# Kernel optimization log

Measured on AMD Instinct MI355X. Metric: run time of the kernel, lower is better.

The kernel has to match this reference:

```python
import jax, jax.numpy as jnp
import numpy as np

B, P = 32, 1024
HID, H, D = 512, 8, 64   # hidden_dim, heads, head_dim
MEM, RANK = 64, 64


def setup_inputs() -> dict:
    key = jax.random.key(0)
    ks = jax.random.split(key, 12)
    s1 = 1.0  # Linear(1, hidden): fan_in = 1 -> torch init bound = 1
    sh = 1.0 / np.sqrt(HID)
    sd = 1.0 / np.sqrt(D)
    return {
        "x":    jax.random.normal(ks[0], (B, P), dtype=jnp.float32),
        # q/k/v: Linear(1, hidden) -> weight (hidden,), bias (hidden,)
        "w_q": jax.random.uniform(ks[1], (HID,), jnp.float32, -s1, s1),
        "b_q": jax.random.uniform(ks[2], (HID,), jnp.float32, -s1, s1),
        "w_k": jax.random.uniform(ks[3], (HID,), jnp.float32, -s1, s1),
        "b_k": jax.random.uniform(ks[4], (HID,), jnp.float32, -s1, s1),
        "w_v": jax.random.uniform(ks[5], (HID,), jnp.float32, -s1, s1),
        "b_v": jax.random.uniform(ks[6], (HID,), jnp.float32, -s1, s1),
        # mem_proj: Linear(head_dim, mem_size, bias=False) -> weight (mem, d)
        "w_mem": jax.random.uniform(ks[7], (MEM, D), jnp.float32, -sd, sd),
        # project_to_U / V: Linear(hidden, rank)
        "w_u":  jax.random.uniform(ks[8], (RANK, HID), jnp.float32, -sh, sh),
        "b_u":  jax.random.uniform(ks[9], (RANK,), jnp.float32, -sh, sh),
        "w_v2": jax.random.uniform(ks[10], (RANK, HID), jnp.float32, -sh, sh),
        "b_v2": jax.random.uniform(ks[11], (RANK,), jnp.float32, -sh, sh),
    }


def reference(x, w_q, b_q, w_k, b_k, w_v, b_v, w_mem, w_u, b_u, w_v2, b_v2):
    Bx, p = x.shape
    xu = x[..., None]                                  # (B, p, 1)
    # Linear(1, hidden) is a scalar broadcast: x * w + b
    def to_heads(w, b):
        y = xu * w + b                                 # (B, p, HID)
        return y.reshape(Bx, p, H, D).transpose(0, 2, 1, 3)  # (B, H, p, D)
    Q = to_heads(w_q, b_q)
    K = to_heads(w_k, b_k)
    V = to_heads(w_v, b_v)

    phi = lambda u: jax.nn.elu(u) + 1.0
    Qf = phi(Q)                                        # (B, H, p, D)
    # memory weights: softmax over the p axis (dim=2)
    W_mem = jax.nn.softmax(jnp.einsum('bhpd,md->bhpm', K, w_mem), axis=2)
    mem_KV = jnp.einsum('bhpm,bhpd->bhmd', W_mem, V)   # (B, H, MEM, D)
    attn = jnp.einsum('bhpd,bhmd->bhpm', Qf, mem_KV)   # (B, H, p, MEM)
    h = jnp.einsum('bhpm,bhmd->bhpd', attn, mem_KV)    # (B, H, p, D)
    h = h.transpose(0, 2, 1, 3).reshape(Bx, p, H * D)  # (B, p, HID)

    U = h @ w_u.T + b_u                                # (B, p, RANK)
    Vp = h @ w_v2.T + b_v2                             # (B, p, RANK)
    coeffs_k = jnp.einsum('bpr,bqr->bpq', U, Vp)       # (B, p, p)
    return coeffs_k
```

## Files before the change

### kernel.cpp

```cpp
#include <hip/hip_runtime.h>
#include <hip/hip_bf16.h>

#define BB 32
#define PP 1024
#define HID 512
#define NH 8
#define DD 64
#define MEM 64
#define RANK 64

typedef float f32x4 __attribute__((ext_vector_type(4)));

#define M_OFF   512
#define G_OFF   18432

__global__ __launch_bounds__(1024) void k_fused(
    const float* __restrict__ x, const float* __restrict__ wq,
    const float* __restrict__ bq, const float* __restrict__ wk,
    const float* __restrict__ wv, const float* __restrict__ bv,
    const float* __restrict__ wmem, const float* __restrict__ wu,
    const float* __restrict__ bu, const float* __restrict__ wv2,
    const float* __restrict__ bv2, float* __restrict__ G,
    float* __restrict__ M17) {
  const int t = threadIdx.x;

  if (blockIdx.x == 256) {
    __shared__ float WU[17 * 64];
    __shared__ float WVt[64 * 17];
    const int r = t >> 4;
    const int dq = t & 15;
    for (int j = 0; j < 17; ++j) {
      float su, sv;
      if (j < 16) {
        const int hh = j & 7;
        const float4 w4 = (j < 8) ? *(const float4*)&wv[hh * DD + dq * 4]
                                  : *(const float4*)&bv[hh * DD + dq * 4];
        const float4 u4 = *(const float4*)&wu[r * HID + hh * DD + dq * 4];
        const float4 v4 = *(const float4*)&wv2[r * HID + hh * DD + dq * 4];
        su = u4.x * w4.x + u4.y * w4.y + u4.z * w4.z + u4.w * w4.w;
        sv = v4.x * w4.x + v4.y * w4.y + v4.z * w4.z + v4.w * w4.w;
      } else {
        su = (dq == 0) ? bu[r] : 0.f;
        sv = (dq == 0) ? bv2[r] : 0.f;
      }
      su += __shfl_xor(su, 1); su += __shfl_xor(su, 2);
      su += __shfl_xor(su, 4); su += __shfl_xor(su, 8);
      sv += __shfl_xor(sv, 1); sv += __shfl_xor(sv, 2);
      sv += __shfl_xor(sv, 4); sv += __shfl_xor(sv, 8);
      if (dq == 0) {
        WU[j * 64 + r] = su;
        WVt[r * 17 + j] = sv;
      }
    }
    __syncthreads();
    if (t < 17 * 17) {
      const int ii = t / 17, jj = t - ii * 17;
      float s = 0.f;
      for (int rr = 0; rr < 64; ++rr) s += WU[ii * 64 + rr] * WVt[rr * 17 + jj];
      M17[t] = s;
    }
    return;
  }

  __shared__ float Tl[MEM];
  __shared__ float sS1, sS2;
  const int b = blockIdx.x >> 3;
  const int h = blockIdx.x & 7;
  const int w = t >> 6;
  const int lane = t & 63;
  const float* xr = x + b * PP;

  const float xv = xr[t];

  float xs[16];
#pragma unroll
  for (int k = 0; k < 16; ++k) xs[k] = xr[lane + k * 64];

  for (int mi = 0; mi < 4; ++mi) {
    const int m = w * 4 + mi;
    float a = wk[h * DD + lane] * wmem[m * DD + lane];
#pragma unroll
    for (int off = 32; off >= 1; off >>= 1) a += __shfl_xor(a, off);

    float mx = -INFINITY;
#pragma unroll
    for (int k = 0; k < 16; ++k) mx = fmaxf(mx, xs[k] * a);
#pragma unroll
    for (int off = 32; off >= 1; off >>= 1) mx = fmaxf(mx, __shfl_xor(mx, off));

    float s = 0.f, sx = 0.f;
#pragma unroll
    for (int k = 0; k < 16; ++k) {
      const float e = __expf(xs[k] * a - mx);
      s += e;
      sx += e * xs[k];
    }
#pragma unroll
    for (int off = 32; off >= 1; off >>= 1) {
      s += __shfl_xor(s, off);
      sx += __shfl_xor(sx, off);
    }
    if (lane == 0) Tl[m] = sx / s;
  }
  __syncthreads();

  if (t < 64) {
    const float v = Tl[t];
    float s1 = v, s2 = v * v;
#pragma unroll
    for (int off = 32; off >= 1; off >>= 1) {
      s1 += __shfl_xor(s1, off);
      s2 += __shfl_xor(s2, off);
    }
    if (t == 0) { sS1 = s1; sS2 = s2; }
  }
  __syncthreads();

  float a1 = 0.f, a0 = 0.f;
#pragma unroll 8
  for (int d = 0; d < DD; ++d) {
    const float q = xv * wq[h * DD + d] + bq[h * DD + d];
    const float ph = (q > 0.f) ? (q + 1.f) : __expf(q);
    a1 += ph * wv[h * DD + d];
    a0 += ph * bv[h * DD + d];
  }
  const float s1 = sS1, s2 = sS2;
  const float c1 = a1 * s2 + a0 * s1;
  const float c2 = a1 * s1 + a0 * (float)MEM;
  G[(b * 16 + h) * PP + t] = c1;
  G[(b * 16 + 8 + h) * PP + t] = c2;
}

__global__ __launch_bounds__(256) void k_coeffs(
    const float* __restrict__ G, const float* __restrict__ M17,
    float* __restrict__ out) {
  __shared__ float Ml[17 * 17];
  __shared__ float Gp[16 * 128];
  __shared__ float Gq[16 * 128];
  __shared__ float Fl[17 * 128];
  const int b = blockIdx.z;
  const int p0 = blockIdx.y * 128;
  const int q0 = blockIdx.x * 128;
  const int t = threadIdx.x;
  const float* Gg = G + (size_t)b * 16 * PP;

  for (int i = t; i < 17 * 17; i += 256) Ml[i] = M17[i];
  for (int i = t; i < 16 * 128; i += 256) {
    const int row = i >> 7, col = i & 127;
    Gp[i] = Gg[row * PP + p0 + col];
    Gq[i] = Gg[row * PP + q0 + col];
  }
  __syncthreads();

  for (int i = t; i < 17 * 128; i += 256) {
    const int j = i >> 7, pp = i & 127;
    float f = Ml[16 * 17 + j];
#pragma unroll
    for (int ii = 0; ii < 16; ++ii) f += Gp[ii * 128 + pp] * Ml[ii * 17 + j];
    Fl[i] = f;
  }
  __syncthreads();

  const int pr = t >> 4;
  const int qv = t & 15;

  float acc[8][8];
#pragma unroll
  for (int r = 0; r < 8; ++r) {
    const float f16 = Fl[16 * 128 + pr * 8 + r];
#pragma unroll
    for (int c = 0; c < 8; ++c) acc[r][c] = f16;
  }

#pragma unroll
  for (int j = 0; j < 16; ++j) {
    const float4 fj0 = *(const float4*)&Fl[j * 128 + pr * 8];
    const float4 fj1 = *(const float4*)&Fl[j * 128 + pr * 8 + 4];
    const float4 gj0 = *(const float4*)&Gq[j * 128 + qv * 8];
    const float4 gj1 = *(const float4*)&Gq[j * 128 + qv * 8 + 4];
    const float fr[8] = {fj0.x, fj0.y, fj0.z, fj0.w, fj1.x, fj1.y, fj1.z, fj1.w};
    const float gc[8] = {gj0.x, gj0.y, gj0.z, gj0.w, gj1.x, gj1.y, gj1.z, gj1.w};
#pragma unroll
    for (int r = 0; r < 8; ++r) {
#pragma unroll
      for (int c = 0; c < 8; ++c) acc[r][c] += fr[r] * gc[c];
    }
  }

  const size_t base = ((size_t)b * PP + p0 + pr * 8) * PP + q0 + qv * 8;
#pragma unroll
  for (int r = 0; r < 8; ++r) {
    const f32x4 v0 = {acc[r][0], acc[r][1], acc[r][2], acc[r][3]};
    const f32x4 v1 = {acc[r][4], acc[r][5], acc[r][6], acc[r][7]};
    __builtin_nontemporal_store(v0, (f32x4*)&out[base + (size_t)r * PP]);
    __builtin_nontemporal_store(v1, (f32x4*)&out[base + (size_t)r * PP + 4]);
  }
}

extern "C" void kernel_launch(void* const* d_in, const int* in_sizes, int n_in,
                              void* d_out, int out_size, void* d_ws, size_t ws_size,
                              hipStream_t stream) {
  const float* x    = (const float*)d_in[0];
  const float* wq   = (const float*)d_in[1];
  const float* bq   = (const float*)d_in[2];
  const float* wk   = (const float*)d_in[3];
  const float* bk   = (const float*)d_in[4];  (void)bk;
  const float* wv   = (const float*)d_in[5];
  const float* bv   = (const float*)d_in[6];
  const float* wmem = (const float*)d_in[7];
  const float* wu   = (const float*)d_in[8];
  const float* bu   = (const float*)d_in[9];
  const float* wv2  = (const float*)d_in[10];
  const float* bv2  = (const float*)d_in[11];

  float* ws = (float*)d_ws;
  float* M17 = ws + M_OFF;
  float* G   = ws + G_OFF;
  float* out = (float*)d_out;

  k_fused<<<257, 1024, 0, stream>>>(x, wq, bq, wk, wv, bv, wmem, wu, bu,
                                    wv2, bv2, G, M17);
  k_coeffs<<<dim3(8, 8, 32), 256, 0, stream>>>(G, M17, out);
}
```

Measured before the change: 210.7 us.

## Loop each coeffs block over four q-tiles with double-buffered G prefetch

Each k_coeffs block now covers four consecutive 128-column q tiles instead of one, so the grid drops from 8x8x32 to 2x8x32. The F projection for the p rows is computed once and reused across the four tiles. While the current tile computes and stores, the next G tile is loaded from global memory into registers and written to a second shared buffer, synchronised with a raw barrier. This cuts the redundant F work and the per-block setup, at the cost of fewer blocks to fill the GPU and more shared memory per block.

```diff
diff --git a/kernel.cpp b/kernel.cpp
--- a/kernel.cpp
+++ b/kernel.cpp
@@ -135,20 +135,21 @@
     const float* __restrict__ G, const float* __restrict__ M17,
     float* __restrict__ out) {
   __shared__ float Ml[17 * 17];
-  __shared__ float Gp[16 * 128];
-  __shared__ float Gq[16 * 128];
-  __shared__ float Fl[17 * 128];
+  __shared__ alignas(16) float Fp[17 * 128];
+  __shared__ alignas(16) float Gp[16 * 128];
+  __shared__ alignas(16) float Gq[2][16 * 128];
   const int b = blockIdx.z;
   const int p0 = blockIdx.y * 128;
-  const int q0 = blockIdx.x * 128;
+  const int qbase = blockIdx.x * 512;
   const int t = threadIdx.x;
   const float* Gg = G + (size_t)b * 16 * PP;
+  const f32x4* Gg4 = (const f32x4*)Gg;
 
   for (int i = t; i < 17 * 17; i += 256) Ml[i] = M17[i];
   for (int i = t; i < 16 * 128; i += 256) {
     const int row = i >> 7, col = i & 127;
     Gp[i] = Gg[row * PP + p0 + col];
-    Gq[i] = Gg[row * PP + q0 + col];
+    Gq[0][i] = Gg[row * PP + qbase + col];
   }
   __syncthreads();
 
@@ -157,43 +158,65 @@
     float f = Ml[16 * 17 + j];
 #pragma unroll
     for (int ii = 0; ii < 16; ++ii) f += Gp[ii * 128 + pp] * Ml[ii * 17 + j];
-    Fl[i] = f;
+    Fp[i] = f;
   }
   __syncthreads();
 
   const int pr = t >> 4;
   const int qv = t & 15;
-
-  float acc[8][8];
-#pragma unroll
-  for (int r = 0; r < 8; ++r) {
-    const float f16 = Fl[16 * 128 + pr * 8 + r];
-#pragma unroll
-    for (int c = 0; c < 8; ++c) acc[r][c] = f16;
-  }
-
-#pragma unroll
-  for (int j = 0; j < 16; ++j) {
-    const float4 fj0 = *(const float4*)&Fl[j * 128 + pr * 8];
-    const float4 fj1 = *(const float4*)&Fl[j * 128 + pr * 8 + 4];
-    const float4 gj0 = *(const float4*)&Gq[j * 128 + qv * 8];
-    const float4 gj1 = *(const float4*)&Gq[j * 128 + qv * 8 + 4];
-    const float fr[8] = {fj0.x, fj0.y, fj0.z, fj0.w, fj1.x, fj1.y, fj1.z, fj1.w};
-    const float gc[8] = {gj0.x, gj0.y, gj0.z, gj0.w, gj1.x, gj1.y, gj1.z, gj1.w};
+  const int e0r = t >> 5, ec = t & 31;
+
+  for (int qt = 0; qt < 4; ++qt) {
+    const int cur = qt & 1, nxt = cur ^ 1;
+    const bool more = (qt < 3);
+    f32x4 pf0, pf1;
+    if (more) {
+      const int q4 = (qbase + (qt + 1) * 128) >> 2;
+      pf0 = Gg4[e0r * 256 + q4 + ec];
+      pf1 = Gg4[(e0r + 8) * 256 + q4 + ec];
+    }
+
+    float acc[8][8];
 #pragma unroll
     for (int r = 0; r < 8; ++r) {
-#pragma unroll
-      for (int c = 0; c < 8; ++c) acc[r][c] += fr[r] * gc[c];
-    }
-  }
-
-  const size_t base = ((size_t)b * PP + p0 + pr * 8) * PP + q0 + qv * 8;
-#pragma unroll
-  for (int r = 0; r < 8; ++r) {
-    const f32x4 v0 = {acc[r][0], acc[r][1], acc[r][2], acc[r][3]};
-    const f32x4 v1 = {acc[r][4], acc[r][5], acc[r][6], acc[r][7]};
-    __builtin_nontemporal_store(v0, (f32x4*)&out[base + (size_t)r * PP]);
-    __builtin_nontemporal_store(v1, (f32x4*)&out[base + (size_t)r * PP + 4]);
+      const float f16 = Fp[16 * 128 + pr * 8 + r];
+#pragma unroll
+      for (int c = 0; c < 8; ++c) acc[r][c] = f16;
+    }
+
+#pragma unroll
+    for (int j = 0; j < 16; ++j) {
+      const float4 fj0 = *(const float4*)&Fp[j * 128 + pr * 8];
+      const float4 fj1 = *(const float4*)&Fp[j * 128 + pr * 8 + 4];
+      const float4 gj0 = *(const float4*)&Gq[cur][j * 128 + qv * 8];
+      const float4 gj1 = *(const float4*)&Gq[cur][j * 128 + qv * 8 + 4];
+      const float fr[8] = {fj0.x, fj0.y, fj0.z, fj0.w, fj1.x, fj1.y, fj1.z, fj1.w};
+      const float gc[8] = {gj0.x, gj0.y, gj0.z, gj0.w, gj1.x, gj1.y, gj1.z, gj1.w};
+#pragma unroll
+      for (int r = 0; r < 8; ++r) {
+#pragma unroll
+        for (int c = 0; c < 8; ++c) acc[r][c] += fr[r] * gc[c];
+      }
+    }
+
+    const int q0 = qbase + qt * 128;
+    const size_t base = ((size_t)b * PP + p0 + pr * 8) * PP + q0 + qv * 8;
+#pragma unroll
+    for (int r = 0; r < 8; ++r) {
+      const f32x4 v0 = {acc[r][0], acc[r][1], acc[r][2], acc[r][3]};
+      const f32x4 v1 = {acc[r][4], acc[r][5], acc[r][6], acc[r][7]};
+      __builtin_nontemporal_store(v0, (f32x4*)&out[base + (size_t)r * PP]);
+      __builtin_nontemporal_store(v1, (f32x4*)&out[base + (size_t)r * PP + 4]);
+    }
+
+    if (more) {
+      ((f32x4*)&Gq[nxt][0])[t] = pf0;
+      ((f32x4*)&Gq[nxt][0])[t + 256] = pf1;
+      asm volatile("s_waitcnt lgkmcnt(0)" ::: "memory");
+      __builtin_amdgcn_s_barrier();
+      asm volatile("" ::: "memory");
+      __builtin_amdgcn_sched_barrier(0);
+    }
   }
 }
 
@@ -220,5 +243,5 @@
 
   k_fused<<<257, 1024, 0, stream>>>(x, wq, bq, wk, wv, bv, wmem, wu, bu,
                                     wv2, bv2, G, M17);
-  k_coeffs<<<dim3(8, 8, 32), 256, 0, stream>>>(G, M17, out);
+  k_coeffs<<<dim3(2, 8, 32), 256, 0, stream>>>(G, M17, out);
 }
```

Result: slower. 240.4 us (+14.1%).
